# Kernel optimization log

Hardware: AMD Instinct MI355X
Metric: run time of the kernel (lower is better)

The kernel has to match this reference:

```python
import jax, jax.numpy as jnp
import numpy as np

N, D, E, H, K = 16384, 256, 8, 512, 2


def setup_inputs() -> dict:
    key = jax.random.key(0)
    ks = jax.random.split(key, 5)
    inputs = jax.random.normal(ks[0], (N, D), dtype=jnp.float32)
    Wg = jax.random.normal(ks[1], (D, E), dtype=jnp.float32) * 0.05
    w1 = jax.random.normal(ks[2], (E, D, H), dtype=jnp.float32) * 0.05
    b1 = jnp.zeros((E, H), dtype=jnp.float32)
    w2 = jax.random.normal(ks[3], (E, H, D), dtype=jnp.float32) * 0.05
    b2 = jnp.zeros((E, D), dtype=jnp.float32)
    return {"inputs": inputs, "Wg": Wg, "w1": w1, "b1": b1, "w2": w2, "b2": b2}


def reference(inputs, Wg, w1, b1, w2, b2):
    # gate + top-k routing (softmax over the selected logits only, as in the torch code)
    gate_logits = inputs @ Wg                       # [N, E]
    topw, topi = jax.lax.top_k(gate_logits, K)      # [N, K]
    topw = jax.nn.softmax(topw.astype(jnp.float32), axis=1).astype(inputs.dtype)
    # combine weights scattered back into a dense [N, E] matrix (dispatch/combine)
    combine = jnp.zeros((N, E), dtype=inputs.dtype)
    combine = combine.at[jnp.arange(N)[:, None], topi].add(topw)  # [N, E]
    # expert MLP (Linear -> GELU(exact) -> Linear), computed per expert and
    # combined with the sparse routing weights (pool='sum')
    h = jax.nn.gelu(jnp.einsum('nd,edh->neh', inputs, w1) + b1[None], approximate=False)  # [N,E,H]
    y = jnp.einsum('neh,ehd->ned', h, w2) + b2[None]                                      # [N,E,D]
    return jnp.einsum('ne,ned->nd', combine, y)                                           # [N,D]
```

## Files before the change

### kernel.cpp

```cpp
#include <hip/hip_runtime.h>

#define NTOK 16384
#define DIM 256
#define NEXP 8
#define HID 512
#define CAP 5120
#define CSTRIDE 16

typedef unsigned short ushort_t;
typedef short bf16x8 __attribute__((ext_vector_type(8)));
typedef float f32x4 __attribute__((ext_vector_type(4)));

static __device__ __forceinline__ ushort_t f2bf(float f) {
    unsigned int u = __float_as_uint(f);
    unsigned int r = (u + 0x7FFFu + ((u >> 16) & 1u)) >> 16;
    return (ushort_t)r;
}
static __device__ __forceinline__ float bf2f(ushort_t u) {
    unsigned int x = ((unsigned int)u) << 16;
    return __uint_as_float(x);
}
static __device__ __forceinline__ float gelu_fast(float v) {
    float v2 = v * v;
    float u = v * __builtin_fmaf(v2, -0.1029407079f, -2.3022090196f);
    float e = __builtin_amdgcn_exp2f(u);
    return v * __builtin_amdgcn_rcpf(1.0f + e);
}

__global__ void k_transpose(const float* __restrict__ w1, const float* __restrict__ w2,
                            ushort_t* __restrict__ w1t, ushort_t* __restrict__ w2t,
                            int* __restrict__ counts) {
    __shared__ ushort_t tile[64][72];
    if (blockIdx.x == 0 && threadIdx.x < NEXP * CSTRIDE) counts[threadIdx.x] = 0;
    int b = blockIdx.x;
    const float* src; ushort_t* dst; int R, C, e, t;
    if (b < 256) { e = b >> 5; t = b & 31; src = w1; dst = w1t + e * DIM * HID; R = DIM; C = HID; }
    else { b -= 256; e = b >> 5; t = b & 31; src = w2; dst = w2t + e * DIM * HID; R = HID; C = DIM; }
    size_t ebase = (size_t)e * DIM * HID;
    int tilesC = C >> 6;
    int rt = t / tilesC, ct = t % tilesC;
    for (int i = 0; i < 16; i++) {
        int flat = i * 256 + threadIdx.x;
        int lr = flat >> 6, lc = flat & 63;
        tile[lr][lc] = f2bf(src[ebase + (size_t)(rt * 64 + lr) * C + ct * 64 + lc]);
    }
    __syncthreads();
    for (int i = 0; i < 16; i++) {
        int flat = i * 256 + threadIdx.x;
        int lr = flat >> 6, lc = flat & 63;
        dst[(ct * 64 + lr) * R + rt * 64 + lc] = tile[lc][lr];
    }
}

__global__ void k_router(const float* __restrict__ X, const float* __restrict__ Wg,
                         int* counts, int* tok_list, int* inv_idx, float* inv_w,
                         ushort_t* __restrict__ Xb) {
    __shared__ float xs[64][257];
    __shared__ float lg[64][8];
    __shared__ int te0[64], te1[64], lo0[64], lo1[64];
    __shared__ float tw0[64], tw1[64];
    __shared__ int lcnt[NEXP], gbase[NEXP];
    int tid = threadIdx.x;
    int tok0 = blockIdx.x * 64;
    if (tid < NEXP) lcnt[tid] = 0;
    for (int i = 0; i < 8; i++) {
        int flat = i * 256 + tid;
        int r = flat >> 5, c8 = (flat & 31) << 3;
        const float* row = X + (size_t)(tok0 + r) * DIM + c8;
        float4 a = *(const float4*)row;
        float4 b = *(const float4*)(row + 4);
        xs[r][c8 + 0] = a.x; xs[r][c8 + 1] = a.y; xs[r][c8 + 2] = a.z; xs[r][c8 + 3] = a.w;
        xs[r][c8 + 4] = b.x; xs[r][c8 + 5] = b.y; xs[r][c8 + 6] = b.z; xs[r][c8 + 7] = b.w;
    }
    __syncthreads();
    for (int i = 0; i < 8; i++) {
        int flat = i * 256 + tid;
        int r = flat >> 5, c8 = (flat & 31) << 3;
        ushort_t pk[8];
#pragma unroll
        for (int j = 0; j < 8; j++) pk[j] = f2bf(xs[r][c8 + j]);
        *(int4*)(Xb + (size_t)(tok0 + r) * DIM + c8) = *(const int4*)pk;
    }
    int tl = tid & 63, pair = tid >> 6;
    float l0 = 0.f, l1 = 0.f;
    for (int d = 0; d < DIM; d++) {
        float x = xs[tl][d];
        l0 += x * Wg[d * NEXP + 2 * pair];
        l1 += x * Wg[d * NEXP + 2 * pair + 1];
    }
    lg[tl][2 * pair] = l0; lg[tl][2 * pair + 1] = l1;
    __syncthreads();
    if (tid < 64) {
        float best = -1e30f; int bi = 0;
#pragma unroll
        for (int e = 0; e < NEXP; e++) { float v = lg[tid][e]; if (v > best) { best = v; bi = e; } }
        float best2 = -1e30f; int bi2 = 0;
#pragma unroll
        for (int e = 0; e < NEXP; e++) { if (e == bi) continue; float v = lg[tid][e]; if (v > best2) { best2 = v; bi2 = e; } }
        float ed = __expf(best2 - best);
        te0[tid] = bi; te1[tid] = bi2;
        tw0[tid] = 1.0f / (1.0f + ed);
        tw1[tid] = ed / (1.0f + ed);
        lo0[tid] = atomicAdd(&lcnt[bi], 1);
        lo1[tid] = atomicAdd(&lcnt[bi2], 1);
    }
    __syncthreads();
    if (tid < NEXP) gbase[tid] = atomicAdd(&counts[tid * CSTRIDE], lcnt[tid]);
    __syncthreads();
    if (tid < 64) {
        int token = tok0 + tid;
        int e0 = te0[tid], e1 = te1[tid];
        int p0 = gbase[e0] + lo0[tid]; if (p0 >= CAP) p0 = CAP - 1;
        int p1 = gbase[e1] + lo1[tid]; if (p1 >= CAP) p1 = CAP - 1;
        tok_list[e0 * CAP + p0] = token;
        tok_list[e1 * CAP + p1] = token;
        inv_idx[token * 2]     = (e0 << 16) | p0;  inv_w[token * 2]     = tw0[tid];
        inv_idx[token * 2 + 1] = (e1 << 16) | p1;  inv_w[token * 2 + 1] = tw1[tid];
    }
}

__launch_bounds__(512, 4)
__global__ void k_mlp1(const ushort_t* __restrict__ Xb, const ushort_t* __restrict__ w1t,
                       const float* __restrict__ b1,
                       const int* __restrict__ counts, const int* __restrict__ tok_list,
                       ushort_t* __restrict__ hb) {
    __shared__ ushort_t B1[128 * 264];
    int b = blockIdx.x;
    int e = b / 160;
    int rem = b % 160;
    int hq = rem / 40, tile = rem % 40;
    int count = counts[e * CSTRIDE];
    if (count > CAP) count = CAP;
    int t0 = tile * 128;
    if (t0 >= count) return;

    int tid = threadIdx.x;
    int w = tid >> 6, l = tid & 63, ln = l & 15, q = l >> 4;

    const ushort_t* w1te = w1t + (size_t)e * DIM * HID + (size_t)hq * 128 * DIM;
#pragma unroll
    for (int i = 0; i < 8; i++) {
        int flat = i * 512 + tid;
        int hr = flat >> 5, c8 = (flat & 31) << 3;
        *(int4*)(B1 + hr * 264 + c8) = *(const int4*)(w1te + hr * DIM + c8);
    }
    int arow = t0 + 16 * w + ln;
    int ci = (arow < count) ? arow : (count - 1);
    int atok = tok_list[e * CAP + ci];
    const ushort_t* xrow = Xb + (size_t)atok * DIM;
    bf16x8 xf[8];
#pragma unroll
    for (int ks = 0; ks < 8; ks++)
        xf[ks] = *(const bf16x8*)(xrow + ks * 32 + q * 8);
    __syncthreads();

    f32x4 zf = {0.f, 0.f, 0.f, 0.f};
    f32x4 acc[8];
#pragma unroll
    for (int i = 0; i < 8; i++) acc[i] = zf;
#pragma unroll
    for (int ks = 0; ks < 8; ks++) {
        bf16x8 xk = xf[ks];
#pragma unroll
        for (int cf = 0; cf < 8; cf++) {
            bf16x8 wfr = *(const bf16x8*)(B1 + (cf * 16 + ln) * 264 + ks * 32 + q * 8);
            acc[cf] = __builtin_amdgcn_mfma_f32_16x16x32_bf16(wfr, xk, acc[cf], 0, 0, 0);
        }
    }
    size_t hrowbase = ((size_t)e * CAP + t0 + 16 * w + ln) * HID + hq * 128;
#pragma unroll
    for (int cf = 0; cf < 8; cf++) {
        float4 bv = *(const float4*)(b1 + e * HID + hq * 128 + cf * 16 + q * 4);
        ushort4 pk;
        pk.x = f2bf(gelu_fast(acc[cf][0] + bv.x));
        pk.y = f2bf(gelu_fast(acc[cf][1] + bv.y));
        pk.z = f2bf(gelu_fast(acc[cf][2] + bv.z));
        pk.w = f2bf(gelu_fast(acc[cf][3] + bv.w));
        *(ushort4*)(hb + hrowbase + cf * 16 + q * 4) = pk;
    }
}

__launch_bounds__(512, 2)
__global__ void k_mlp2(const ushort_t* __restrict__ hb, const ushort_t* __restrict__ w2t,
                       const float* __restrict__ b2,
                       const int* __restrict__ counts, ushort_t* __restrict__ yb) {
    __shared__ ushort_t B2[64 * 520];
    int b = blockIdx.x;
    int e = b / 160;
    int rem = b % 160;
    int dq = rem / 40, tile = rem % 40;
    int count = counts[e * CSTRIDE];
    if (count > CAP) count = CAP;
    int t0 = tile * 128;
    if (t0 >= count) return;

    int tid = threadIdx.x;
    int w = tid >> 6, l = tid & 63, ln = l & 15, q = l >> 4;

    const ushort_t* w2te = w2t + (size_t)e * DIM * HID + (size_t)dq * 64 * HID;
#pragma unroll
    for (int i = 0; i < 8; i++) {
        int flat = i * 512 + tid;
        int dr = flat >> 6, c8 = (flat & 63) << 3;
        *(int4*)(B2 + dr * 520 + c8) = *(const int4*)(w2te + dr * HID + c8);
    }
    int arow = t0 + 16 * w + ln;
    int ci = (arow < count) ? arow : (count - 1);
    const ushort_t* hrow = hb + ((size_t)e * CAP + ci) * HID;
    bf16x8 af[16];
#pragma unroll
    for (int ks = 0; ks < 16; ks++)
        af[ks] = *(const bf16x8*)(hrow + ks * 32 + q * 8);
    __syncthreads();

    f32x4 zf = {0.f, 0.f, 0.f, 0.f};
    f32x4 acc[4];
#pragma unroll
    for (int i = 0; i < 4; i++) acc[i] = zf;
#pragma unroll
    for (int ks = 0; ks < 16; ks++) {
        bf16x8 hk = af[ks];
#pragma unroll
        for (int cf = 0; cf < 4; cf++) {
            bf16x8 wfr = *(const bf16x8*)(B2 + (cf * 16 + ln) * 520 + ks * 32 + q * 8);
            acc[cf] = __builtin_amdgcn_mfma_f32_16x16x32_bf16(wfr, hk, acc[cf], 0, 0, 0);
        }
    }
    size_t yrowbase = ((size_t)e * CAP + t0 + 16 * w + ln) * DIM + dq * 64;
#pragma unroll
    for (int cf = 0; cf < 4; cf++) {
        float4 bv = *(const float4*)(b2 + e * DIM + dq * 64 + cf * 16 + q * 4);
        ushort4 pk;
        pk.x = f2bf(acc[cf][0] + bv.x);
        pk.y = f2bf(acc[cf][1] + bv.y);
        pk.z = f2bf(acc[cf][2] + bv.z);
        pk.w = f2bf(acc[cf][3] + bv.w);
        *(ushort4*)(yb + yrowbase + cf * 16 + q * 4) = pk;
    }
}

__global__ void k_combine(const ushort_t* __restrict__ yb, const int* __restrict__ inv_idx,
                          const float* __restrict__ inv_w, float* __restrict__ out) {
    int tid = threadIdx.x;
    int n = blockIdx.x * 8 + (tid >> 5);
    int l32 = tid & 31, c8 = l32 << 3;
    int i0 = inv_idx[2 * n], i1 = inv_idx[2 * n + 1];
    float w0 = inv_w[2 * n], w1 = inv_w[2 * n + 1];
    size_t r0 = (size_t)(i0 >> 16) * CAP + (i0 & 0xFFFF);
    size_t r1 = (size_t)(i1 >> 16) * CAP + (i1 & 0xFFFF);
    int4 v0 = *(const int4*)(yb + r0 * DIM + c8);
    int4 v1 = *(const int4*)(yb + r1 * DIM + c8);
    ushort_t* p0 = (ushort_t*)&v0;
    ushort_t* p1 = (ushort_t*)&v1;
    float4 oa, ob;
    oa.x = w0 * bf2f(p0[0]) + w1 * bf2f(p1[0]);
    oa.y = w0 * bf2f(p0[1]) + w1 * bf2f(p1[1]);
    oa.z = w0 * bf2f(p0[2]) + w1 * bf2f(p1[2]);
    oa.w = w0 * bf2f(p0[3]) + w1 * bf2f(p1[3]);
    ob.x = w0 * bf2f(p0[4]) + w1 * bf2f(p1[4]);
    ob.y = w0 * bf2f(p0[5]) + w1 * bf2f(p1[5]);
    ob.z = w0 * bf2f(p0[6]) + w1 * bf2f(p1[6]);
    ob.w = w0 * bf2f(p0[7]) + w1 * bf2f(p1[7]);
    float4* op = (float4*)(out + (size_t)n * DIM + c8);
    op[0] = oa; op[1] = ob;
}

extern "C" void kernel_launch(void* const* d_in, const int* in_sizes, int n_in,
                              void* d_out, int out_size, void* d_ws, size_t ws_size,
                              hipStream_t stream) {
    const float* X  = (const float*)d_in[0];
    const float* Wg = (const float*)d_in[1];
    const float* w1 = (const float*)d_in[2];
    const float* b1 = (const float*)d_in[3];
    const float* w2 = (const float*)d_in[4];
    const float* b2 = (const float*)d_in[5];

    char* ws = (char*)d_ws;
    size_t off = 0;
    int* counts = (int*)(ws + off);        off = 1024;
    int* tok_list = (int*)(ws + off);      off += (size_t)NEXP * CAP * 4;
    int* inv_idx = (int*)(ws + off);       off += (size_t)NTOK * 2 * 4;
    float* inv_w = (float*)(ws + off);     off += (size_t)NTOK * 2 * 4;
    ushort_t* w1t = (ushort_t*)(ws + off); off += (size_t)NEXP * DIM * HID * 2;
    ushort_t* w2t = (ushort_t*)(ws + off); off += (size_t)NEXP * DIM * HID * 2;
    ushort_t* Xb = (ushort_t*)(ws + off);  off += (size_t)NTOK * DIM * 2;
    ushort_t* hb = (ushort_t*)(ws + off);  off += (size_t)NEXP * CAP * HID * 2;
    ushort_t* yb = (ushort_t*)(ws + off);  off += (size_t)NEXP * CAP * DIM * 2;

    k_transpose<<<512, 256, 0, stream>>>(w1, w2, w1t, w2t, counts);
    k_router<<<256, 256, 0, stream>>>(X, Wg, counts, tok_list, inv_idx, inv_w, Xb);
    k_mlp1<<<NEXP * 40 * 4, 512, 0, stream>>>(Xb, w1t, b1, counts, tok_list, hb);
    k_mlp2<<<NEXP * 40 * 4, 512, 0, stream>>>(hb, w2t, b2, counts, yb);
    k_combine<<<2048, 256, 0, stream>>>(yb, inv_idx, inv_w, (float*)d_out);
}
```

Measured before the change: 158.5 us.

## Merge transpose and router kernels; retile expert GEMMs to 256-token tiles

Fuses the weight transpose/cast and router kernels into one launch that shares LDS through a union, and moves the counts reset to a memset. The two expert MLP kernels now give each wave two 16-row token fragments per tile (256 tokens per block), so every weight fragment read from LDS feeds two MFMAs. MLP1 shrinks its hidden slice to 64 and MLP2 raises its occupancy bound. The aim is fewer launches and less LDS traffic per MFMA, at the cost of more registers and more padded work on partial tiles.

```diff
diff --git a/kernel.cpp b/kernel.cpp
--- a/kernel.cpp
+++ b/kernel.cpp
@@ -27,50 +27,57 @@
     return v * __builtin_amdgcn_rcpf(1.0f + e);
 }
 
-__global__ void k_transpose(const float* __restrict__ w1, const float* __restrict__ w2,
-                            ushort_t* __restrict__ w1t, ushort_t* __restrict__ w2t,
-                            int* __restrict__ counts) {
-    __shared__ ushort_t tile[64][72];
-    if (blockIdx.x == 0 && threadIdx.x < NEXP * CSTRIDE) counts[threadIdx.x] = 0;
+struct RouterSmem {
+    float xs[64][257];
+    float lg[64][8];
+    int te0[64], te1[64], lo0[64], lo1[64];
+    float tw0[64], tw1[64];
+    int lcnt[NEXP], gbase[NEXP];
+};
+union PrepSmem {
+    ushort_t tile[64][72];
+    RouterSmem r;
+};
+
+__global__ void k_prep(const float* __restrict__ X, const float* __restrict__ Wg,
+                       const float* __restrict__ w1, const float* __restrict__ w2,
+                       ushort_t* __restrict__ w1t, ushort_t* __restrict__ w2t,
+                       int* counts, int* tok_list, int* inv_idx, float* inv_w,
+                       ushort_t* __restrict__ Xb) {
+    __shared__ PrepSmem sm;
     int b = blockIdx.x;
-    const float* src; ushort_t* dst; int R, C, e, t;
-    if (b < 256) { e = b >> 5; t = b & 31; src = w1; dst = w1t + e * DIM * HID; R = DIM; C = HID; }
-    else { b -= 256; e = b >> 5; t = b & 31; src = w2; dst = w2t + e * DIM * HID; R = HID; C = DIM; }
-    size_t ebase = (size_t)e * DIM * HID;
-    int tilesC = C >> 6;
-    int rt = t / tilesC, ct = t % tilesC;
-    for (int i = 0; i < 16; i++) {
-        int flat = i * 256 + threadIdx.x;
-        int lr = flat >> 6, lc = flat & 63;
-        tile[lr][lc] = f2bf(src[ebase + (size_t)(rt * 64 + lr) * C + ct * 64 + lc]);
-    }
-    __syncthreads();
-    for (int i = 0; i < 16; i++) {
-        int flat = i * 256 + threadIdx.x;
-        int lr = flat >> 6, lc = flat & 63;
-        dst[(ct * 64 + lr) * R + rt * 64 + lc] = tile[lc][lr];
-    }
-}
-
-__global__ void k_router(const float* __restrict__ X, const float* __restrict__ Wg,
-                         int* counts, int* tok_list, int* inv_idx, float* inv_w,
-                         ushort_t* __restrict__ Xb) {
-    __shared__ float xs[64][257];
-    __shared__ float lg[64][8];
-    __shared__ int te0[64], te1[64], lo0[64], lo1[64];
-    __shared__ float tw0[64], tw1[64];
-    __shared__ int lcnt[NEXP], gbase[NEXP];
     int tid = threadIdx.x;
-    int tok0 = blockIdx.x * 64;
-    if (tid < NEXP) lcnt[tid] = 0;
+    if (b < 512) {
+        const float* src; ushort_t* dst; int R, C, e, t;
+        if (b < 256) { e = b >> 5; t = b & 31; src = w1; dst = w1t + e * DIM * HID; R = DIM; C = HID; }
+        else { int bb = b - 256; e = bb >> 5; t = bb & 31; src = w2; dst = w2t + e * DIM * HID; R = HID; C = DIM; }
+        size_t ebase = (size_t)e * DIM * HID;
+        int tilesC = C >> 6;
+        int rt = t / tilesC, ct = t % tilesC;
+        for (int i = 0; i < 16; i++) {
+            int flat = i * 256 + tid;
+            int lr = flat >> 6, lc = flat & 63;
+            sm.tile[lr][lc] = f2bf(src[ebase + (size_t)(rt * 64 + lr) * C + ct * 64 + lc]);
+        }
+        __syncthreads();
+        for (int i = 0; i < 16; i++) {
+            int flat = i * 256 + tid;
+            int lr = flat >> 6, lc = flat & 63;
+            dst[(ct * 64 + lr) * R + rt * 64 + lc] = sm.tile[lc][lr];
+        }
+        return;
+    }
+    b -= 512;
+    int tok0 = b * 64;
+    if (tid < NEXP) sm.r.lcnt[tid] = 0;
     for (int i = 0; i < 8; i++) {
         int flat = i * 256 + tid;
         int r = flat >> 5, c8 = (flat & 31) << 3;
         const float* row = X + (size_t)(tok0 + r) * DIM + c8;
         float4 a = *(const float4*)row;
-        float4 b = *(const float4*)(row + 4);
-        xs[r][c8 + 0] = a.x; xs[r][c8 + 1] = a.y; xs[r][c8 + 2] = a.z; xs[r][c8 + 3] = a.w;
-        xs[r][c8 + 4] = b.x; xs[r][c8 + 5] = b.y; xs[r][c8 + 6] = b.z; xs[r][c8 + 7] = b.w;
+        float4 bb = *(const float4*)(row + 4);
+        sm.r.xs[r][c8 + 0] = a.x; sm.r.xs[r][c8 + 1] = a.y; sm.r.xs[r][c8 + 2] = a.z; sm.r.xs[r][c8 + 3] = a.w;
+        sm.r.xs[r][c8 + 4] = bb.x; sm.r.xs[r][c8 + 5] = bb.y; sm.r.xs[r][c8 + 6] = bb.z; sm.r.xs[r][c8 + 7] = bb.w;
     }
     __syncthreads();
     for (int i = 0; i < 8; i++) {
@@ -78,44 +85,44 @@
         int r = flat >> 5, c8 = (flat & 31) << 3;
         ushort_t pk[8];
 #pragma unroll
-        for (int j = 0; j < 8; j++) pk[j] = f2bf(xs[r][c8 + j]);
+        for (int j = 0; j < 8; j++) pk[j] = f2bf(sm.r.xs[r][c8 + j]);
         *(int4*)(Xb + (size_t)(tok0 + r) * DIM + c8) = *(const int4*)pk;
     }
     int tl = tid & 63, pair = tid >> 6;
     float l0 = 0.f, l1 = 0.f;
     for (int d = 0; d < DIM; d++) {
-        float x = xs[tl][d];
+        float x = sm.r.xs[tl][d];
         l0 += x * Wg[d * NEXP + 2 * pair];
         l1 += x * Wg[d * NEXP + 2 * pair + 1];
     }
-    lg[tl][2 * pair] = l0; lg[tl][2 * pair + 1] = l1;
+    sm.r.lg[tl][2 * pair] = l0; sm.r.lg[tl][2 * pair + 1] = l1;
     __syncthreads();
     if (tid < 64) {
         float best = -1e30f; int bi = 0;
 #pragma unroll
-        for (int e = 0; e < NEXP; e++) { float v = lg[tid][e]; if (v > best) { best = v; bi = e; } }
+        for (int e = 0; e < NEXP; e++) { float v = sm.r.lg[tid][e]; if (v > best) { best = v; bi = e; } }
         float best2 = -1e30f; int bi2 = 0;
 #pragma unroll
-        for (int e = 0; e < NEXP; e++) { if (e == bi) continue; float v = lg[tid][e]; if (v > best2) { best2 = v; bi2 = e; } }
+        for (int e = 0; e < NEXP; e++) { if (e == bi) continue; float v = sm.r.lg[tid][e]; if (v > best2) { best2 = v; bi2 = e; } }
         float ed = __expf(best2 - best);
-        te0[tid] = bi; te1[tid] = bi2;
-        tw0[tid] = 1.0f / (1.0f + ed);
-        tw1[tid] = ed / (1.0f + ed);
-        lo0[tid] = atomicAdd(&lcnt[bi], 1);
-        lo1[tid] = atomicAdd(&lcnt[bi2], 1);
-    }
-    __syncthreads();
-    if (tid < NEXP) gbase[tid] = atomicAdd(&counts[tid * CSTRIDE], lcnt[tid]);
+        sm.r.te0[tid] = bi; sm.r.te1[tid] = bi2;
+        sm.r.tw0[tid] = 1.0f / (1.0f + ed);
+        sm.r.tw1[tid] = ed / (1.0f + ed);
+        sm.r.lo0[tid] = atomicAdd(&sm.r.lcnt[bi], 1);
+        sm.r.lo1[tid] = atomicAdd(&sm.r.lcnt[bi2], 1);
+    }
+    __syncthreads();
+    if (tid < NEXP) sm.r.gbase[tid] = atomicAdd(&counts[tid * CSTRIDE], sm.r.lcnt[tid]);
     __syncthreads();
     if (tid < 64) {
         int token = tok0 + tid;
-        int e0 = te0[tid], e1 = te1[tid];
-        int p0 = gbase[e0] + lo0[tid]; if (p0 >= CAP) p0 = CAP - 1;
-        int p1 = gbase[e1] + lo1[tid]; if (p1 >= CAP) p1 = CAP - 1;
+        int e0 = sm.r.te0[tid], e1 = sm.r.te1[tid];
+        int p0 = sm.r.gbase[e0] + sm.r.lo0[tid]; if (p0 >= CAP) p0 = CAP - 1;
+        int p1 = sm.r.gbase[e1] + sm.r.lo1[tid]; if (p1 >= CAP) p1 = CAP - 1;
         tok_list[e0 * CAP + p0] = token;
         tok_list[e1 * CAP + p1] = token;
-        inv_idx[token * 2]     = (e0 << 16) | p0;  inv_w[token * 2]     = tw0[tid];
-        inv_idx[token * 2 + 1] = (e1 << 16) | p1;  inv_w[token * 2 + 1] = tw1[tid];
+        inv_idx[token * 2]     = (e0 << 16) | p0;  inv_w[token * 2]     = sm.r.tw0[tid];
+        inv_idx[token * 2 + 1] = (e1 << 16) | p1;  inv_w[token * 2 + 1] = sm.r.tw1[tid];
     }
 }
 
@@ -124,74 +131,89 @@
                        const float* __restrict__ b1,
                        const int* __restrict__ counts, const int* __restrict__ tok_list,
                        ushort_t* __restrict__ hb) {
-    __shared__ ushort_t B1[128 * 264];
+    __shared__ ushort_t B1[64 * 264];
     int b = blockIdx.x;
     int e = b / 160;
     int rem = b % 160;
-    int hq = rem / 40, tile = rem % 40;
+    int hq = rem / 20, tile = rem % 20;
     int count = counts[e * CSTRIDE];
     if (count > CAP) count = CAP;
-    int t0 = tile * 128;
+    int t0 = tile * 256;
     if (t0 >= count) return;
 
     int tid = threadIdx.x;
     int w = tid >> 6, l = tid & 63, ln = l & 15, q = l >> 4;
 
-    const ushort_t* w1te = w1t + (size_t)e * DIM * HID + (size_t)hq * 128 * DIM;
-#pragma unroll
-    for (int i = 0; i < 8; i++) {
+    const ushort_t* w1te = w1t + (size_t)e * DIM * HID + (size_t)hq * 64 * DIM;
+#pragma unroll
+    for (int i = 0; i < 4; i++) {
         int flat = i * 512 + tid;
         int hr = flat >> 5, c8 = (flat & 31) << 3;
         *(int4*)(B1 + hr * 264 + c8) = *(const int4*)(w1te + hr * DIM + c8);
     }
-    int arow = t0 + 16 * w + ln;
-    int ci = (arow < count) ? arow : (count - 1);
-    int atok = tok_list[e * CAP + ci];
-    const ushort_t* xrow = Xb + (size_t)atok * DIM;
-    bf16x8 xf[8];
-#pragma unroll
-    for (int ks = 0; ks < 8; ks++)
-        xf[ks] = *(const bf16x8*)(xrow + ks * 32 + q * 8);
+    int arow0 = t0 + 32 * w + ln;
+    int arow1 = arow0 + 16;
+    int ci0 = (arow0 < count) ? arow0 : (count - 1);
+    int ci1 = (arow1 < count) ? arow1 : (count - 1);
+    int tk0 = tok_list[e * CAP + ci0];
+    int tk1 = tok_list[e * CAP + ci1];
+    const ushort_t* xr0 = Xb + (size_t)tk0 * DIM;
+    const ushort_t* xr1 = Xb + (size_t)tk1 * DIM;
     __syncthreads();
 
     f32x4 zf = {0.f, 0.f, 0.f, 0.f};
-    f32x4 acc[8];
-#pragma unroll
-    for (int i = 0; i < 8; i++) acc[i] = zf;
-#pragma unroll
-    for (int ks = 0; ks < 8; ks++) {
-        bf16x8 xk = xf[ks];
-#pragma unroll
-        for (int cf = 0; cf < 8; cf++) {
-            bf16x8 wfr = *(const bf16x8*)(B1 + (cf * 16 + ln) * 264 + ks * 32 + q * 8);
-            acc[cf] = __builtin_amdgcn_mfma_f32_16x16x32_bf16(wfr, xk, acc[cf], 0, 0, 0);
-        }
-    }
-    size_t hrowbase = ((size_t)e * CAP + t0 + 16 * w + ln) * HID + hq * 128;
-#pragma unroll
-    for (int cf = 0; cf < 8; cf++) {
-        float4 bv = *(const float4*)(b1 + e * HID + hq * 128 + cf * 16 + q * 4);
-        ushort4 pk;
-        pk.x = f2bf(gelu_fast(acc[cf][0] + bv.x));
-        pk.y = f2bf(gelu_fast(acc[cf][1] + bv.y));
-        pk.z = f2bf(gelu_fast(acc[cf][2] + bv.z));
-        pk.w = f2bf(gelu_fast(acc[cf][3] + bv.w));
-        *(ushort4*)(hb + hrowbase + cf * 16 + q * 4) = pk;
-    }
-}
-
-__launch_bounds__(512, 2)
+    f32x4 acc[4][2];
+#pragma unroll
+    for (int i = 0; i < 4; i++) { acc[i][0] = zf; acc[i][1] = zf; }
+#pragma unroll
+    for (int kk = 0; kk < 2; kk++) {
+        bf16x8 xf0[4], xf1[4];
+#pragma unroll
+        for (int ks = 0; ks < 4; ks++) {
+            xf0[ks] = *(const bf16x8*)(xr0 + kk * 128 + ks * 32 + q * 8);
+            xf1[ks] = *(const bf16x8*)(xr1 + kk * 128 + ks * 32 + q * 8);
+        }
+#pragma unroll
+        for (int ks = 0; ks < 4; ks++) {
+#pragma unroll
+            for (int cf = 0; cf < 4; cf++) {
+                bf16x8 wfr = *(const bf16x8*)(B1 + (cf * 16 + ln) * 264 + kk * 128 + ks * 32 + q * 8);
+                acc[cf][0] = __builtin_amdgcn_mfma_f32_16x16x32_bf16(wfr, xf0[ks], acc[cf][0], 0, 0, 0);
+                acc[cf][1] = __builtin_amdgcn_mfma_f32_16x16x32_bf16(wfr, xf1[ks], acc[cf][1], 0, 0, 0);
+            }
+        }
+    }
+    size_t base0 = ((size_t)e * CAP + arow0) * HID + hq * 64;
+    size_t base1 = ((size_t)e * CAP + arow1) * HID + hq * 64;
+#pragma unroll
+    for (int cf = 0; cf < 4; cf++) {
+        float4 bv = *(const float4*)(b1 + e * HID + hq * 64 + cf * 16 + q * 4);
+        ushort4 pk0, pk1;
+        pk0.x = f2bf(gelu_fast(acc[cf][0][0] + bv.x));
+        pk0.y = f2bf(gelu_fast(acc[cf][0][1] + bv.y));
+        pk0.z = f2bf(gelu_fast(acc[cf][0][2] + bv.z));
+        pk0.w = f2bf(gelu_fast(acc[cf][0][3] + bv.w));
+        pk1.x = f2bf(gelu_fast(acc[cf][1][0] + bv.x));
+        pk1.y = f2bf(gelu_fast(acc[cf][1][1] + bv.y));
+        pk1.z = f2bf(gelu_fast(acc[cf][1][2] + bv.z));
+        pk1.w = f2bf(gelu_fast(acc[cf][1][3] + bv.w));
+        *(ushort4*)(hb + base0 + cf * 16 + q * 4) = pk0;
+        *(ushort4*)(hb + base1 + cf * 16 + q * 4) = pk1;
+    }
+}
+
+__launch_bounds__(512, 4)
 __global__ void k_mlp2(const ushort_t* __restrict__ hb, const ushort_t* __restrict__ w2t,
                        const float* __restrict__ b2,
                        const int* __restrict__ counts, ushort_t* __restrict__ yb) {
     __shared__ ushort_t B2[64 * 520];
     int b = blockIdx.x;
-    int e = b / 160;
-    int rem = b % 160;
-    int dq = rem / 40, tile = rem % 40;
+    int e = b / 80;
+    int rem = b % 80;
+    int dq = rem / 20, tile = rem % 20;
     int count = counts[e * CSTRIDE];
     if (count > CAP) count = CAP;
-    int t0 = tile * 128;
+    int t0 = tile * 256;
     if (t0 >= count) return;
 
     int tid = threadIdx.x;
@@ -204,38 +226,52 @@
         int dr = flat >> 6, c8 = (flat & 63) << 3;
         *(int4*)(B2 + dr * 520 + c8) = *(const int4*)(w2te + dr * HID + c8);
     }
-    int arow = t0 + 16 * w + ln;
-    int ci = (arow < count) ? arow : (count - 1);
-    const ushort_t* hrow = hb + ((size_t)e * CAP + ci) * HID;
-    bf16x8 af[16];
-#pragma unroll
-    for (int ks = 0; ks < 16; ks++)
-        af[ks] = *(const bf16x8*)(hrow + ks * 32 + q * 8);
+    int arow0 = t0 + 32 * w + ln;
+    int arow1 = arow0 + 16;
+    int ci0 = (arow0 < count) ? arow0 : (count - 1);
+    int ci1 = (arow1 < count) ? arow1 : (count - 1);
+    const ushort_t* hr0 = hb + ((size_t)e * CAP + ci0) * HID;
+    const ushort_t* hr1 = hb + ((size_t)e * CAP + ci1) * HID;
     __syncthreads();
 
     f32x4 zf = {0.f, 0.f, 0.f, 0.f};
-    f32x4 acc[4];
-#pragma unroll
-    for (int i = 0; i < 4; i++) acc[i] = zf;
-#pragma unroll
-    for (int ks = 0; ks < 16; ks++) {
-        bf16x8 hk = af[ks];
-#pragma unroll
-        for (int cf = 0; cf < 4; cf++) {
-            bf16x8 wfr = *(const bf16x8*)(B2 + (cf * 16 + ln) * 520 + ks * 32 + q * 8);
-            acc[cf] = __builtin_amdgcn_mfma_f32_16x16x32_bf16(wfr, hk, acc[cf], 0, 0, 0);
-        }
-    }
-    size_t yrowbase = ((size_t)e * CAP + t0 + 16 * w + ln) * DIM + dq * 64;
+    f32x4 acc[4][2];
+#pragma unroll
+    for (int i = 0; i < 4; i++) { acc[i][0] = zf; acc[i][1] = zf; }
+#pragma unroll
+    for (int kk = 0; kk < 4; kk++) {
+        bf16x8 hf0[4], hf1[4];
+#pragma unroll
+        for (int ks = 0; ks < 4; ks++) {
+            hf0[ks] = *(const bf16x8*)(hr0 + kk * 128 + ks * 32 + q * 8);
+            hf1[ks] = *(const bf16x8*)(hr1 + kk * 128 + ks * 32 + q * 8);
+        }
+#pragma unroll
+        for (int ks = 0; ks < 4; ks++) {
+#pragma unroll
+            for (int cf = 0; cf < 4; cf++) {
+                bf16x8 wfr = *(const bf16x8*)(B2 + (cf * 16 + ln) * 520 + kk * 128 + ks * 32 + q * 8);
+                acc[cf][0] = __builtin_amdgcn_mfma_f32_16x16x32_bf16(wfr, hf0[ks], acc[cf][0], 0, 0, 0);
+                acc[cf][1] = __builtin_amdgcn_mfma_f32_16x16x32_bf16(wfr, hf1[ks], acc[cf][1], 0, 0, 0);
+            }
+        }
+    }
+    size_t yb0 = ((size_t)e * CAP + arow0) * DIM + dq * 64;
+    size_t yb1 = ((size_t)e * CAP + arow1) * DIM + dq * 64;
 #pragma unroll
     for (int cf = 0; cf < 4; cf++) {
         float4 bv = *(const float4*)(b2 + e * DIM + dq * 64 + cf * 16 + q * 4);
-        ushort4 pk;
-        pk.x = f2bf(acc[cf][0] + bv.x);
-        pk.y = f2bf(acc[cf][1] + bv.y);
-        pk.z = f2bf(acc[cf][2] + bv.z);
-        pk.w = f2bf(acc[cf][3] + bv.w);
-        *(ushort4*)(yb + yrowbase + cf * 16 + q * 4) = pk;
+        ushort4 pk0, pk1;
+        pk0.x = f2bf(acc[cf][0][0] + bv.x);
+        pk0.y = f2bf(acc[cf][0][1] + bv.y);
+        pk0.z = f2bf(acc[cf][0][2] + bv.z);
+        pk0.w = f2bf(acc[cf][0][3] + bv.w);
+        pk1.x = f2bf(acc[cf][1][0] + bv.x);
+        pk1.y = f2bf(acc[cf][1][1] + bv.y);
+        pk1.z = f2bf(acc[cf][1][2] + bv.z);
+        pk1.w = f2bf(acc[cf][1][3] + bv.w);
+        *(ushort4*)(yb + yb0 + cf * 16 + q * 4) = pk0;
+        *(ushort4*)(yb + yb1 + cf * 16 + q * 4) = pk1;
     }
 }
 
@@ -287,9 +323,9 @@
     ushort_t* hb = (ushort_t*)(ws + off);  off += (size_t)NEXP * CAP * HID * 2;
     ushort_t* yb = (ushort_t*)(ws + off);  off += (size_t)NEXP * CAP * DIM * 2;
 
-    k_transpose<<<512, 256, 0, stream>>>(w1, w2, w1t, w2t, counts);
-    k_router<<<256, 256, 0, stream>>>(X, Wg, counts, tok_list, inv_idx, inv_w, Xb);
-    k_mlp1<<<NEXP * 40 * 4, 512, 0, stream>>>(Xb, w1t, b1, counts, tok_list, hb);
-    k_mlp2<<<NEXP * 40 * 4, 512, 0, stream>>>(hb, w2t, b2, counts, yb);
+    hipMemsetAsync(counts, 0, 1024, stream);
+    k_prep<<<768, 256, 0, stream>>>(X, Wg, w1, w2, w1t, w2t, counts, tok_list, inv_idx, inv_w, Xb);
+    k_mlp1<<<NEXP * 8 * 20, 512, 0, stream>>>(Xb, w1t, b1, counts, tok_list, hb);
+    k_mlp2<<<NEXP * 4 * 20, 512, 0, stream>>>(hb, w2t, b2, counts, yb);
     k_combine<<<2048, 256, 0, stream>>>(yb, inv_idx, inv_w, (float*)d_out);
 }
```

Result: slower. 168.3 us (+6.2%).

## Loop output quarters inside MLP blocks and halve router tokens per block

Applied to the files above, without the earlier changes.

The MLP kernels no longer spread the four hidden/output quarters across separate blocks. Each block now loads its token rows once into registers and loops over the four weight quarters, restaging shared memory each time, so the gathered activation loads are not repeated four times. The router uses 32 tokens per block with one expert per thread, doubling its grid, and k_mlp2 launch bounds rise to 4 blocks per CU. The trade-off is a quarter as many MLP blocks (up to 320), which may leave the GPU underfilled, and weight staging is now serialized with compute inside each block.

```diff
diff --git a/kernel.cpp b/kernel.cpp
--- a/kernel.cpp
+++ b/kernel.cpp
@@ -55,15 +55,15 @@
 __global__ void k_router(const float* __restrict__ X, const float* __restrict__ Wg,
                          int* counts, int* tok_list, int* inv_idx, float* inv_w,
                          ushort_t* __restrict__ Xb) {
-    __shared__ float xs[64][257];
-    __shared__ float lg[64][8];
-    __shared__ int te0[64], te1[64], lo0[64], lo1[64];
-    __shared__ float tw0[64], tw1[64];
+    __shared__ float xs[32][257];
+    __shared__ float lg[32][8];
+    __shared__ int te0[32], te1[32], lo0[32], lo1[32];
+    __shared__ float tw0[32], tw1[32];
     __shared__ int lcnt[NEXP], gbase[NEXP];
     int tid = threadIdx.x;
-    int tok0 = blockIdx.x * 64;
+    int tok0 = blockIdx.x * 32;
     if (tid < NEXP) lcnt[tid] = 0;
-    for (int i = 0; i < 8; i++) {
+    for (int i = 0; i < 4; i++) {
         int flat = i * 256 + tid;
         int r = flat >> 5, c8 = (flat & 31) << 3;
         const float* row = X + (size_t)(tok0 + r) * DIM + c8;
@@ -73,7 +73,7 @@
         xs[r][c8 + 4] = b.x; xs[r][c8 + 5] = b.y; xs[r][c8 + 6] = b.z; xs[r][c8 + 7] = b.w;
     }
     __syncthreads();
-    for (int i = 0; i < 8; i++) {
+    for (int i = 0; i < 4; i++) {
         int flat = i * 256 + tid;
         int r = flat >> 5, c8 = (flat & 31) << 3;
         ushort_t pk[8];
@@ -81,16 +81,12 @@
         for (int j = 0; j < 8; j++) pk[j] = f2bf(xs[r][c8 + j]);
         *(int4*)(Xb + (size_t)(tok0 + r) * DIM + c8) = *(const int4*)pk;
     }
-    int tl = tid & 63, pair = tid >> 6;
-    float l0 = 0.f, l1 = 0.f;
-    for (int d = 0; d < DIM; d++) {
-        float x = xs[tl][d];
-        l0 += x * Wg[d * NEXP + 2 * pair];
-        l1 += x * Wg[d * NEXP + 2 * pair + 1];
-    }
-    lg[tl][2 * pair] = l0; lg[tl][2 * pair + 1] = l1;
-    __syncthreads();
-    if (tid < 64) {
+    int tl = tid & 31, ex = tid >> 5;
+    float acc = 0.f;
+    for (int d = 0; d < DIM; d++) acc += xs[tl][d] * Wg[d * NEXP + ex];
+    lg[tl][ex] = acc;
+    __syncthreads();
+    if (tid < 32) {
         float best = -1e30f; int bi = 0;
 #pragma unroll
         for (int e = 0; e < NEXP; e++) { float v = lg[tid][e]; if (v > best) { best = v; bi = e; } }
@@ -107,7 +103,7 @@
     __syncthreads();
     if (tid < NEXP) gbase[tid] = atomicAdd(&counts[tid * CSTRIDE], lcnt[tid]);
     __syncthreads();
-    if (tid < 64) {
+    if (tid < 32) {
         int token = tok0 + tid;
         int e0 = te0[tid], e1 = te1[tid];
         int p0 = gbase[e0] + lo0[tid]; if (p0 >= CAP) p0 = CAP - 1;
@@ -126,9 +122,8 @@
                        ushort_t* __restrict__ hb) {
     __shared__ ushort_t B1[128 * 264];
     int b = blockIdx.x;
-    int e = b / 160;
-    int rem = b % 160;
-    int hq = rem / 40, tile = rem % 40;
+    int e = b / 40;
+    int tile = b % 40;
     int count = counts[e * CSTRIDE];
     if (count > CAP) count = CAP;
     int t0 = tile * 128;
@@ -137,13 +132,6 @@
     int tid = threadIdx.x;
     int w = tid >> 6, l = tid & 63, ln = l & 15, q = l >> 4;
 
-    const ushort_t* w1te = w1t + (size_t)e * DIM * HID + (size_t)hq * 128 * DIM;
-#pragma unroll
-    for (int i = 0; i < 8; i++) {
-        int flat = i * 512 + tid;
-        int hr = flat >> 5, c8 = (flat & 31) << 3;
-        *(int4*)(B1 + hr * 264 + c8) = *(const int4*)(w1te + hr * DIM + c8);
-    }
     int arow = t0 + 16 * w + ln;
     int ci = (arow < count) ? arow : (count - 1);
     int atok = tok_list[e * CAP + ci];
@@ -152,43 +140,54 @@
 #pragma unroll
     for (int ks = 0; ks < 8; ks++)
         xf[ks] = *(const bf16x8*)(xrow + ks * 32 + q * 8);
-    __syncthreads();
-
-    f32x4 zf = {0.f, 0.f, 0.f, 0.f};
-    f32x4 acc[8];
-#pragma unroll
-    for (int i = 0; i < 8; i++) acc[i] = zf;
-#pragma unroll
-    for (int ks = 0; ks < 8; ks++) {
-        bf16x8 xk = xf[ks];
+
+    const ushort_t* w1te = w1t + (size_t)e * DIM * HID;
+    size_t hrowbase = ((size_t)e * CAP + t0 + 16 * w + ln) * HID;
+
+    for (int hq = 0; hq < 4; hq++) {
+        __syncthreads();
+#pragma unroll
+        for (int i = 0; i < 8; i++) {
+            int flat = i * 512 + tid;
+            int hr = flat >> 5, c8 = (flat & 31) << 3;
+            *(int4*)(B1 + hr * 264 + c8) = *(const int4*)(w1te + (size_t)(hq * 128 + hr) * DIM + c8);
+        }
+        __syncthreads();
+
+        f32x4 zf = {0.f, 0.f, 0.f, 0.f};
+        f32x4 acc[8];
+#pragma unroll
+        for (int i = 0; i < 8; i++) acc[i] = zf;
+#pragma unroll
+        for (int ks = 0; ks < 8; ks++) {
+            bf16x8 xk = xf[ks];
+#pragma unroll
+            for (int cf = 0; cf < 8; cf++) {
+                bf16x8 wfr = *(const bf16x8*)(B1 + (cf * 16 + ln) * 264 + ks * 32 + q * 8);
+                acc[cf] = __builtin_amdgcn_mfma_f32_16x16x32_bf16(wfr, xk, acc[cf], 0, 0, 0);
+            }
+        }
 #pragma unroll
         for (int cf = 0; cf < 8; cf++) {
-            bf16x8 wfr = *(const bf16x8*)(B1 + (cf * 16 + ln) * 264 + ks * 32 + q * 8);
-            acc[cf] = __builtin_amdgcn_mfma_f32_16x16x32_bf16(wfr, xk, acc[cf], 0, 0, 0);
-        }
-    }
-    size_t hrowbase = ((size_t)e * CAP + t0 + 16 * w + ln) * HID + hq * 128;
-#pragma unroll
-    for (int cf = 0; cf < 8; cf++) {
-        float4 bv = *(const float4*)(b1 + e * HID + hq * 128 + cf * 16 + q * 4);
-        ushort4 pk;
-        pk.x = f2bf(gelu_fast(acc[cf][0] + bv.x));
-        pk.y = f2bf(gelu_fast(acc[cf][1] + bv.y));
-        pk.z = f2bf(gelu_fast(acc[cf][2] + bv.z));
-        pk.w = f2bf(gelu_fast(acc[cf][3] + bv.w));
-        *(ushort4*)(hb + hrowbase + cf * 16 + q * 4) = pk;
-    }
-}
-
-__launch_bounds__(512, 2)
+            float4 bv = *(const float4*)(b1 + e * HID + hq * 128 + cf * 16 + q * 4);
+            ushort4 pk;
+            pk.x = f2bf(gelu_fast(acc[cf][0] + bv.x));
+            pk.y = f2bf(gelu_fast(acc[cf][1] + bv.y));
+            pk.z = f2bf(gelu_fast(acc[cf][2] + bv.z));
+            pk.w = f2bf(gelu_fast(acc[cf][3] + bv.w));
+            *(ushort4*)(hb + hrowbase + hq * 128 + cf * 16 + q * 4) = pk;
+        }
+    }
+}
+
+__launch_bounds__(512, 4)
 __global__ void k_mlp2(const ushort_t* __restrict__ hb, const ushort_t* __restrict__ w2t,
                        const float* __restrict__ b2,
                        const int* __restrict__ counts, ushort_t* __restrict__ yb) {
     __shared__ ushort_t B2[64 * 520];
     int b = blockIdx.x;
-    int e = b / 160;
-    int rem = b % 160;
-    int dq = rem / 40, tile = rem % 40;
+    int e = b / 40;
+    int tile = b % 40;
     int count = counts[e * CSTRIDE];
     if (count > CAP) count = CAP;
     int t0 = tile * 128;
@@ -197,13 +196,6 @@
     int tid = threadIdx.x;
     int w = tid >> 6, l = tid & 63, ln = l & 15, q = l >> 4;
 
-    const ushort_t* w2te = w2t + (size_t)e * DIM * HID + (size_t)dq * 64 * HID;
-#pragma unroll
-    for (int i = 0; i < 8; i++) {
-        int flat = i * 512 + tid;
-        int dr = flat >> 6, c8 = (flat & 63) << 3;
-        *(int4*)(B2 + dr * 520 + c8) = *(const int4*)(w2te + dr * HID + c8);
-    }
     int arow = t0 + 16 * w + ln;
     int ci = (arow < count) ? arow : (count - 1);
     const ushort_t* hrow = hb + ((size_t)e * CAP + ci) * HID;
@@ -211,31 +203,43 @@
 #pragma unroll
     for (int ks = 0; ks < 16; ks++)
         af[ks] = *(const bf16x8*)(hrow + ks * 32 + q * 8);
-    __syncthreads();
-
-    f32x4 zf = {0.f, 0.f, 0.f, 0.f};
-    f32x4 acc[4];
-#pragma unroll
-    for (int i = 0; i < 4; i++) acc[i] = zf;
-#pragma unroll
-    for (int ks = 0; ks < 16; ks++) {
-        bf16x8 hk = af[ks];
+
+    const ushort_t* w2te = w2t + (size_t)e * DIM * HID;
+    size_t yrowbase = ((size_t)e * CAP + t0 + 16 * w + ln) * DIM;
+
+    for (int dq = 0; dq < 4; dq++) {
+        __syncthreads();
+#pragma unroll
+        for (int i = 0; i < 8; i++) {
+            int flat = i * 512 + tid;
+            int dr = flat >> 6, c8 = (flat & 63) << 3;
+            *(int4*)(B2 + dr * 520 + c8) = *(const int4*)(w2te + (size_t)(dq * 64 + dr) * HID + c8);
+        }
+        __syncthreads();
+
+        f32x4 zf = {0.f, 0.f, 0.f, 0.f};
+        f32x4 acc[4];
+#pragma unroll
+        for (int i = 0; i < 4; i++) acc[i] = zf;
+#pragma unroll
+        for (int ks = 0; ks < 16; ks++) {
+            bf16x8 hk = af[ks];
+#pragma unroll
+            for (int cf = 0; cf < 4; cf++) {
+                bf16x8 wfr = *(const bf16x8*)(B2 + (cf * 16 + ln) * 520 + ks * 32 + q * 8);
+                acc[cf] = __builtin_amdgcn_mfma_f32_16x16x32_bf16(wfr, hk, acc[cf], 0, 0, 0);
+            }
+        }
 #pragma unroll
         for (int cf = 0; cf < 4; cf++) {
-            bf16x8 wfr = *(const bf16x8*)(B2 + (cf * 16 + ln) * 520 + ks * 32 + q * 8);
-            acc[cf] = __builtin_amdgcn_mfma_f32_16x16x32_bf16(wfr, hk, acc[cf], 0, 0, 0);
-        }
-    }
-    size_t yrowbase = ((size_t)e * CAP + t0 + 16 * w + ln) * DIM + dq * 64;
-#pragma unroll
-    for (int cf = 0; cf < 4; cf++) {
-        float4 bv = *(const float4*)(b2 + e * DIM + dq * 64 + cf * 16 + q * 4);
-        ushort4 pk;
-        pk.x = f2bf(acc[cf][0] + bv.x);
-        pk.y = f2bf(acc[cf][1] + bv.y);
-        pk.z = f2bf(acc[cf][2] + bv.z);
-        pk.w = f2bf(acc[cf][3] + bv.w);
-        *(ushort4*)(yb + yrowbase + cf * 16 + q * 4) = pk;
+            float4 bv = *(const float4*)(b2 + e * DIM + dq * 64 + cf * 16 + q * 4);
+            ushort4 pk;
+            pk.x = f2bf(acc[cf][0] + bv.x);
+            pk.y = f2bf(acc[cf][1] + bv.y);
+            pk.z = f2bf(acc[cf][2] + bv.z);
+            pk.w = f2bf(acc[cf][3] + bv.w);
+            *(ushort4*)(yb + yrowbase + dq * 64 + cf * 16 + q * 4) = pk;
+        }
     }
 }
 
@@ -288,8 +292,8 @@
     ushort_t* yb = (ushort_t*)(ws + off);  off += (size_t)NEXP * CAP * DIM * 2;
 
     k_transpose<<<512, 256, 0, stream>>>(w1, w2, w1t, w2t, counts);
-    k_router<<<256, 256, 0, stream>>>(X, Wg, counts, tok_list, inv_idx, inv_w, Xb);
-    k_mlp1<<<NEXP * 40 * 4, 512, 0, stream>>>(Xb, w1t, b1, counts, tok_list, hb);
-    k_mlp2<<<NEXP * 40 * 4, 512, 0, stream>>>(hb, w2t, b2, counts, yb);
+    k_router<<<512, 256, 0, stream>>>(X, Wg, counts, tok_list, inv_idx, inv_w, Xb);
+    k_mlp1<<<NEXP * 40, 512, 0, stream>>>(Xb, w1t, b1, counts, tok_list, hb);
+    k_mlp2<<<NEXP * 40, 512, 0, stream>>>(hb, w2t, b2, counts, yb);
     k_combine<<<2048, 256, 0, stream>>>(yb, inv_idx, inv_w, (float*)d_out);
 }
```

Result: slower. 183.8 us (+16.0%).

## Fuse expert MLP layers into one kernel streaming hidden chunks through LDS

Applied to the files above, without the earlier changes.

Merges the two expert GEMM kernels into one. Each 64-token tile loops over the hidden dimension in chunks of 32. Per chunk it loads W1 and W2 slices into LDS, computes GELU(xW1+b1) into an LDS buffer, and accumulates the second GEMM in registers. This removes the global round trip of the bf16 hidden activation and one kernel launch. In exchange, every block reloads the full expert weights from L2, adds two barriers per chunk with little MFMA work between them, and holds 16 accumulator tiles per lane, which raises register pressure.

```diff
diff --git a/kernel.cpp b/kernel.cpp
--- a/kernel.cpp
+++ b/kernel.cpp
@@ -6,6 +6,8 @@
 #define HID 512
 #define CAP 5120
 #define CSTRIDE 16
+#define HC 32
+#define A2S 40
 
 typedef unsigned short ushort_t;
 typedef short bf16x8 __attribute__((ext_vector_type(8)));
@@ -26,6 +28,7 @@
     float e = __builtin_amdgcn_exp2f(u);
     return v * __builtin_amdgcn_rcpf(1.0f + e);
 }
+#define PIN(x) asm volatile("" : "+v"(x))
 
 __global__ void k_transpose(const float* __restrict__ w1, const float* __restrict__ w2,
                             ushort_t* __restrict__ w1t, ushort_t* __restrict__ w2t,
@@ -119,31 +122,26 @@
     }
 }
 
-__launch_bounds__(512, 4)
-__global__ void k_mlp1(const ushort_t* __restrict__ Xb, const ushort_t* __restrict__ w1t,
-                       const float* __restrict__ b1,
-                       const int* __restrict__ counts, const int* __restrict__ tok_list,
-                       ushort_t* __restrict__ hb) {
-    __shared__ ushort_t B1[128 * 264];
+__launch_bounds__(256, 3)
+__global__ void k_mlp_fused(const ushort_t* __restrict__ Xb,
+                            const ushort_t* __restrict__ w1t, const float* __restrict__ b1,
+                            const ushort_t* __restrict__ w2t, const float* __restrict__ b2,
+                            const int* __restrict__ counts, const int* __restrict__ tok_list,
+                            ushort_t* __restrict__ yb) {
+    __shared__ ushort_t A1[HC * 264];
+    __shared__ ushort_t A2[DIM * A2S];
+    __shared__ ushort_t HB[64 * A2S];
     int b = blockIdx.x;
-    int e = b / 160;
-    int rem = b % 160;
-    int hq = rem / 40, tile = rem % 40;
+    int e = b / 80;
+    int tile = b % 80;
     int count = counts[e * CSTRIDE];
     if (count > CAP) count = CAP;
-    int t0 = tile * 128;
+    int t0 = tile * 64;
     if (t0 >= count) return;
 
     int tid = threadIdx.x;
     int w = tid >> 6, l = tid & 63, ln = l & 15, q = l >> 4;
 
-    const ushort_t* w1te = w1t + (size_t)e * DIM * HID + (size_t)hq * 128 * DIM;
-#pragma unroll
-    for (int i = 0; i < 8; i++) {
-        int flat = i * 512 + tid;
-        int hr = flat >> 5, c8 = (flat & 31) << 3;
-        *(int4*)(B1 + hr * 264 + c8) = *(const int4*)(w1te + hr * DIM + c8);
-    }
     int arow = t0 + 16 * w + ln;
     int ci = (arow < count) ? arow : (count - 1);
     int atok = tok_list[e * CAP + ci];
@@ -152,90 +150,72 @@
 #pragma unroll
     for (int ks = 0; ks < 8; ks++)
         xf[ks] = *(const bf16x8*)(xrow + ks * 32 + q * 8);
-    __syncthreads();
+#pragma unroll
+    for (int ks = 0; ks < 8; ks++) PIN(xf[ks]);
+
+    const ushort_t* w1te = w1t + (size_t)e * DIM * HID;
+    const ushort_t* w2te = w2t + (size_t)e * DIM * HID;
 
     f32x4 zf = {0.f, 0.f, 0.f, 0.f};
-    f32x4 acc[8];
-#pragma unroll
-    for (int i = 0; i < 8; i++) acc[i] = zf;
-#pragma unroll
-    for (int ks = 0; ks < 8; ks++) {
-        bf16x8 xk = xf[ks];
-#pragma unroll
-        for (int cf = 0; cf < 8; cf++) {
-            bf16x8 wfr = *(const bf16x8*)(B1 + (cf * 16 + ln) * 264 + ks * 32 + q * 8);
-            acc[cf] = __builtin_amdgcn_mfma_f32_16x16x32_bf16(wfr, xk, acc[cf], 0, 0, 0);
-        }
-    }
-    size_t hrowbase = ((size_t)e * CAP + t0 + 16 * w + ln) * HID + hq * 128;
-#pragma unroll
-    for (int cf = 0; cf < 8; cf++) {
-        float4 bv = *(const float4*)(b1 + e * HID + hq * 128 + cf * 16 + q * 4);
+    f32x4 yacc[16];
+#pragma unroll
+    for (int i = 0; i < 16; i++) yacc[i] = zf;
+
+    for (int ic = 0; ic < 16; ic++) {
+        int hc = ic * HC;
+        __syncthreads();
+#pragma unroll
+        for (int i = 0; i < 4; i++) {
+            int flat = i * 256 + tid;
+            int hr = flat >> 5, c8 = (flat & 31) << 3;
+            *(int4*)(A1 + hr * 264 + c8) = *(const int4*)(w1te + (size_t)(hc + hr) * DIM + c8);
+        }
+#pragma unroll
+        for (int i = 0; i < 4; i++) {
+            int flat = i * 256 + tid;
+            int dr = flat >> 2, c8 = (flat & 3) << 3;
+            *(int4*)(A2 + dr * A2S + c8) = *(const int4*)(w2te + (size_t)dr * HID + hc + c8);
+        }
+        __syncthreads();
+
+        f32x4 hacc[2];
+        hacc[0] = zf; hacc[1] = zf;
+#pragma unroll
+        for (int ks = 0; ks < 8; ks++) {
+            bf16x8 xk = xf[ks];
+#pragma unroll
+            for (int cf = 0; cf < 2; cf++) {
+                bf16x8 wfr = *(const bf16x8*)(A1 + (cf * 16 + ln) * 264 + ks * 32 + q * 8);
+                hacc[cf] = __builtin_amdgcn_mfma_f32_16x16x32_bf16(wfr, xk, hacc[cf], 0, 0, 0);
+            }
+        }
+#pragma unroll
+        for (int cf = 0; cf < 2; cf++) {
+            float4 bv = *(const float4*)(b1 + e * HID + hc + cf * 16 + q * 4);
+            ushort4 pk;
+            pk.x = f2bf(gelu_fast(hacc[cf][0] + bv.x));
+            pk.y = f2bf(gelu_fast(hacc[cf][1] + bv.y));
+            pk.z = f2bf(gelu_fast(hacc[cf][2] + bv.z));
+            pk.w = f2bf(gelu_fast(hacc[cf][3] + bv.w));
+            *(ushort4*)(HB + (16 * w + ln) * A2S + cf * 16 + q * 4) = pk;
+        }
+        bf16x8 hf = *(const bf16x8*)(HB + (16 * w + ln) * A2S + q * 8);
+#pragma unroll
+        for (int cf2 = 0; cf2 < 16; cf2++) {
+            bf16x8 wfr2 = *(const bf16x8*)(A2 + (cf2 * 16 + ln) * A2S + q * 8);
+            yacc[cf2] = __builtin_amdgcn_mfma_f32_16x16x32_bf16(wfr2, hf, yacc[cf2], 0, 0, 0);
+        }
+    }
+    size_t yrowbase = ((size_t)e * CAP + arow) * DIM;
+#pragma unroll
+    for (int cf2 = 0; cf2 < 16; cf2++) {
+        float4 bv = *(const float4*)(b2 + e * DIM + cf2 * 16 + q * 4);
         ushort4 pk;
-        pk.x = f2bf(gelu_fast(acc[cf][0] + bv.x));
-        pk.y = f2bf(gelu_fast(acc[cf][1] + bv.y));
-        pk.z = f2bf(gelu_fast(acc[cf][2] + bv.z));
-        pk.w = f2bf(gelu_fast(acc[cf][3] + bv.w));
-        *(ushort4*)(hb + hrowbase + cf * 16 + q * 4) = pk;
-    }
-}
-
-__launch_bounds__(512, 2)
-__global__ void k_mlp2(const ushort_t* __restrict__ hb, const ushort_t* __restrict__ w2t,
-                       const float* __restrict__ b2,
-                       const int* __restrict__ counts, ushort_t* __restrict__ yb) {
-    __shared__ ushort_t B2[64 * 520];
-    int b = blockIdx.x;
-    int e = b / 160;
-    int rem = b % 160;
-    int dq = rem / 40, tile = rem % 40;
-    int count = counts[e * CSTRIDE];
-    if (count > CAP) count = CAP;
-    int t0 = tile * 128;
-    if (t0 >= count) return;
-
-    int tid = threadIdx.x;
-    int w = tid >> 6, l = tid & 63, ln = l & 15, q = l >> 4;
-
-    const ushort_t* w2te = w2t + (size_t)e * DIM * HID + (size_t)dq * 64 * HID;
-#pragma unroll
-    for (int i = 0; i < 8; i++) {
-        int flat = i * 512 + tid;
-        int dr = flat >> 6, c8 = (flat & 63) << 3;
-        *(int4*)(B2 + dr * 520 + c8) = *(const int4*)(w2te + dr * HID + c8);
-    }
-    int arow = t0 + 16 * w + ln;
-    int ci = (arow < count) ? arow : (count - 1);
-    const ushort_t* hrow = hb + ((size_t)e * CAP + ci) * HID;
-    bf16x8 af[16];
-#pragma unroll
-    for (int ks = 0; ks < 16; ks++)
-        af[ks] = *(const bf16x8*)(hrow + ks * 32 + q * 8);
-    __syncthreads();
-
-    f32x4 zf = {0.f, 0.f, 0.f, 0.f};
-    f32x4 acc[4];
-#pragma unroll
-    for (int i = 0; i < 4; i++) acc[i] = zf;
-#pragma unroll
-    for (int ks = 0; ks < 16; ks++) {
-        bf16x8 hk = af[ks];
-#pragma unroll
-        for (int cf = 0; cf < 4; cf++) {
-            bf16x8 wfr = *(const bf16x8*)(B2 + (cf * 16 + ln) * 520 + ks * 32 + q * 8);
-            acc[cf] = __builtin_amdgcn_mfma_f32_16x16x32_bf16(wfr, hk, acc[cf], 0, 0, 0);
-        }
-    }
-    size_t yrowbase = ((size_t)e * CAP + t0 + 16 * w + ln) * DIM + dq * 64;
-#pragma unroll
-    for (int cf = 0; cf < 4; cf++) {
-        float4 bv = *(const float4*)(b2 + e * DIM + dq * 64 + cf * 16 + q * 4);
-        ushort4 pk;
-        pk.x = f2bf(acc[cf][0] + bv.x);
-        pk.y = f2bf(acc[cf][1] + bv.y);
-        pk.z = f2bf(acc[cf][2] + bv.z);
-        pk.w = f2bf(acc[cf][3] + bv.w);
-        *(ushort4*)(yb + yrowbase + cf * 16 + q * 4) = pk;
+        pk.x = f2bf(yacc[cf2][0] + bv.x);
+        pk.y = f2bf(yacc[cf2][1] + bv.y);
+        pk.z = f2bf(yacc[cf2][2] + bv.z);
+        pk.w = f2bf(yacc[cf2][3] + bv.w);
+        *(ushort4*)(yb + yrowbase + cf2 * 16 + q * 4) = pk;
     }
 }
 
@@ -284,12 +264,10 @@
     ushort_t* w1t = (ushort_t*)(ws + off); off += (size_t)NEXP * DIM * HID * 2;
     ushort_t* w2t = (ushort_t*)(ws + off); off += (size_t)NEXP * DIM * HID * 2;
     ushort_t* Xb = (ushort_t*)(ws + off);  off += (size_t)NTOK * DIM * 2;
-    ushort_t* hb = (ushort_t*)(ws + off);  off += (size_t)NEXP * CAP * HID * 2;
     ushort_t* yb = (ushort_t*)(ws + off);  off += (size_t)NEXP * CAP * DIM * 2;
 
     k_transpose<<<512, 256, 0, stream>>>(w1, w2, w1t, w2t, counts);
     k_router<<<256, 256, 0, stream>>>(X, Wg, counts, tok_list, inv_idx, inv_w, Xb);
-    k_mlp1<<<NEXP * 40 * 4, 512, 0, stream>>>(Xb, w1t, b1, counts, tok_list, hb);
-    k_mlp2<<<NEXP * 40 * 4, 512, 0, stream>>>(hb, w2t, b2, counts, yb);
+    k_mlp_fused<<<NEXP * 80, 256, 0, stream>>>(Xb, w1t, b1, w2t, b2, counts, tok_list, yb);
     k_combine<<<2048, 256, 0, stream>>>(yb, inv_idx, inv_w, (float*)d_out);
 }
```

Result: faster. 153.4 us (-3.2%).
